# Kernel tuning notes

Measured on AMD Instinct MI355X. Metric: run time of the kernel, lower is better.

## Reference

```python
import jax, jax.numpy as jnp
import numpy as np

N_NODES = 100000
N_EDGES = 1600000
IN_DIM, HID_DIM, OUT_DIM = 128, 256, 512
BN_EPS = 1e-5


def setup_inputs() -> dict:
    key = jax.random.key(0)
    ks = jax.random.split(key, 10)
    x = jax.random.normal(ks[0], (N_NODES, IN_DIM), dtype=jnp.float32)
    edge_index = jax.random.randint(ks[1], (2, N_EDGES), 0, N_NODES, dtype=jnp.int64)
    def lin(k, o, i):
        return jax.random.normal(k, (o, i), dtype=jnp.float32) * (1.0 / np.sqrt(i))
    return {
        "x": x,
        "edge_index": edge_index,
        # SAGEConv 1: in_dim -> hidden_dim (lin_l has bias, lin_r has none)
        "W1l": lin(ks[2], HID_DIM, IN_DIM),
        "b1": jnp.zeros((HID_DIM,), dtype=jnp.float32),
        "W1r": lin(ks[3], HID_DIM, IN_DIM),
        # BatchNorm1d(hidden_dim)
        "gamma": jnp.ones((HID_DIM,), dtype=jnp.float32),
        "beta": jnp.zeros((HID_DIM,), dtype=jnp.float32),
        # SAGEConv 2: hidden_dim -> gnn_out_dim
        "W2l": lin(ks[4], OUT_DIM, HID_DIM),
        "b2": jnp.zeros((OUT_DIM,), dtype=jnp.float32),
        "W2r": lin(ks[5], OUT_DIM, HID_DIM),
    }


def _sage_max(h, src, dst, Wl, b, Wr, n_nodes):
    # gather source features, max-aggregate onto destination nodes
    agg = jax.ops.segment_max(h[src], dst, num_segments=n_nodes)  # [N, D]
    agg = jnp.where(jnp.isneginf(agg), 0.0, agg)  # PyG fills empty segments with 0
    return agg @ Wl.T + b + h @ Wr.T


def reference(x, edge_index, W1l, b1, W1r, gamma, beta, W2l, b2, W2r):
    src, dst = edge_index[0], edge_index[1]
    n = x.shape[0]
    # layer 1: SAGEConv(in_dim, hidden_dim, aggr='max')
    h = _sage_max(x, src, dst, W1l, b1, W1r, n)
    # BatchNorm1d (batch statistics), Dropout is identity in eval; no activation in 'sage' branch
    mean = jnp.mean(h, axis=0)
    var = jnp.var(h, axis=0)
    h = gamma * (h - mean) * jax.lax.rsqrt(var + BN_EPS) + beta
    # layer 2: SAGEConv(hidden_dim, gnn_out_dim, aggr='max')
    out = _sage_max(h, src, dst, W2l, b2, W2r, n)
    return out
```

## Files before the change

kernel.cpp:

```cpp
#include <hip/hip_runtime.h>
#include <hip/hip_bf16.h>
#include <stdint.h>

#define N_NODES 100000
#define N_EDGES 1600000
#define IN_DIM 128
#define HID_DIM 256
#define OUT_DIM 512
#define NBUK 391
#define BCAP 8192
#define EPB 4096

typedef __attribute__((ext_vector_type(4))) float f32x4;
typedef __attribute__((ext_vector_type(8))) short bf16x8;

__device__ __forceinline__ float bf16lo(uint32_t u){ uint32_t b = u << 16; return __builtin_bit_cast(float, b); }
__device__ __forceinline__ float bf16hi(uint32_t u){ uint32_t b = u & 0xffff0000u; return __builtin_bit_cast(float, b); }
__device__ __forceinline__ uint16_t f32_to_bf16(float f){
  uint32_t u = __builtin_bit_cast(uint32_t, f);
  uint32_t r = (u + 0x7fffu + ((u >> 16) & 1u)) >> 16;
  return (uint16_t)r;
}
__device__ __forceinline__ uint32_t pack_bf16_exact(float lo, float hi){
  return (__builtin_bit_cast(uint32_t, hi) & 0xffff0000u) | (__builtin_bit_cast(uint32_t, lo) >> 16);
}
__device__ __forceinline__ uint32_t pack_bf16_rne(float lo, float hi){
  return (uint32_t)f32_to_bf16(lo) | ((uint32_t)f32_to_bf16(hi) << 16);
}
__device__ __forceinline__ void gl2lds16(const void* g, void* l){
  __builtin_amdgcn_global_load_lds(
      (const __attribute__((address_space(1))) uint32_t*)g,
      (__attribute__((address_space(3))) uint32_t*)l, 16, 0, 0);
}

__global__ void k_convx(const float* __restrict__ x, uint16_t* __restrict__ X1x,
                        int* __restrict__ gcur, float* __restrict__ sum,
                        float* __restrict__ sumsq){
  if (blockIdx.x == 12500){
    const int t = threadIdx.x;
    for (int i = t; i < NBUK; i += 256) gcur[i] = i << 13;
    sum[t] = 0.f; sumsq[t] = 0.f;
    return;
  }
  const int idx = blockIdx.x * 256 + threadIdx.x;
  const int n = idx >> 5, q = idx & 31;
  const float4 v = *(const float4*)(x + (long)n * 128 + q * 4);
  ushort4 o;
  o.x = f32_to_bf16(v.x); o.y = f32_to_bf16(v.y);
  o.z = f32_to_bf16(v.z); o.w = f32_to_bf16(v.w);
  *(ushort4*)(X1x + (long)n * 128 + q * 4) = o;
}

__global__ void k_bucket(const int* __restrict__ src, const int* __restrict__ dst,
                         int* __restrict__ gcur, int* __restrict__ ebuk){
  __shared__ int hist[NBUK], curs[NBUK], base[NBUK];
  const int tid = threadIdx.x;
  const int e0 = blockIdx.x * EPB;
  for (int t = tid; t < NBUK; t += 256) hist[t] = 0;
  __syncthreads();
  for (int i = 0; i < EPB; i += 256){
    int e = e0 + i + tid;
    if (e < N_EDGES) atomicAdd(&hist[dst[e] >> 8], 1);
  }
  __syncthreads();
  for (int t = tid; t < NBUK; t += 256){
    int h = hist[t];
    base[t] = h ? atomicAdd(&gcur[t], h) : 0;
    curs[t] = 0;
  }
  __syncthreads();
  for (int i = 0; i < EPB; i += 256){
    int e = e0 + i + tid;
    if (e < N_EDGES){
      int d = dst[e];
      int b = d >> 8;
      int idx = atomicAdd(&curs[b], 1);
      int pos = base[b] + idx;
      if (pos < ((b + 1) << 13))
        ebuk[pos] = ((d & 255) << 17) | src[e];
    }
  }
}

__global__ __launch_bounds__(256)
void k_fillc(const int* __restrict__ gcur, const int* __restrict__ ebuk,
             int* __restrict__ row_start, int* __restrict__ esrc){
  __shared__ int ebuf[BCAP];
  __shared__ int cnt[256];
  __shared__ int wtot[4];
  __shared__ int red[4];
  const int b = blockIdx.x, tid = threadIdx.x, lane = tid & 63, wv = tid >> 6;
  const int nodebase = b << 8;
  const int nodecnt = min(256, N_NODES - nodebase);
  int accb = 0;
  for (int t = tid; t < b; t += 256) accb += gcur[t] - (t << 13);
  #pragma unroll
  for (int d = 32; d > 0; d >>= 1) accb += __shfl_xor(accb, d);
  if (lane == 0) red[wv] = accb;
  int size_b = gcur[b] - (b << 13);
  if (size_b > BCAP) size_b = BCAP;
  cnt[tid] = 0;
  for (int i = tid; i < size_b; i += 256) ebuf[i] = ebuk[(b << 13) + i];
  __syncthreads();
  const int bs = red[0] + red[1] + red[2] + red[3];
  for (int i = tid; i < size_b; i += 256) atomicAdd(&cnt[ebuf[i] >> 17], 1);
  __syncthreads();
  const int c = cnt[tid];
  int v = c;
  #pragma unroll
  for (int d = 1; d < 64; d <<= 1){ int t = __shfl_up(v, d); if (lane >= d) v += t; }
  if (lane == 63) wtot[wv] = v;
  __syncthreads();
  if (tid < 4){
    int t = wtot[tid];
    #pragma unroll
    for (int d = 1; d < 4; d <<= 1){ int u = __shfl_up(t, d); if (tid >= d) t += u; }
    wtot[tid] = t;
  }
  __syncthreads();
  const int excl = (wv ? wtot[wv - 1] : 0) + (v - c);
  if (tid < nodecnt) row_start[nodebase + tid] = bs + excl;
  if (b == NBUK - 1 && tid == 0) row_start[N_NODES] = N_EDGES;
  cnt[tid] = excl;
  __syncthreads();
  for (int i = tid; i < size_b; i += 256){
    int p = ebuf[i];
    int pos = atomicAdd(&cnt[p >> 17], 1);
    esrc[bs + pos] = p & 0x1FFFF;
  }
}

__global__ void k_w1(const float* __restrict__ W1l, const float* __restrict__ W1r,
                     uint16_t* __restrict__ W1cat){
  int idx = blockIdx.x * 256 + threadIdx.x;
  int j = idx >> 8, k = idx & 255;
  float v = (k < 128) ? W1l[j * 128 + k] : W1r[j * 128 + (k - 128)];
  W1cat[idx] = f32_to_bf16(v);
}

__global__ void k_w2(const float* __restrict__ W2l, const float* __restrict__ W2r,
                     const float* __restrict__ b2, const float* __restrict__ sum,
                     const float* __restrict__ sumsq, const float* __restrict__ gamma,
                     const float* __restrict__ beta, uint16_t* __restrict__ W2cat,
                     float* __restrict__ bias2, float* __restrict__ scale_g,
                     float* __restrict__ shift_g){
  __shared__ float sc_s[256], sh_s[256];
  const int tid = threadIdx.x;
  {
    const float inv_n = 1.0f / (float)N_NODES;
    float mean = sum[tid] * inv_n;
    float var = sumsq[tid] * inv_n - mean * mean;
    float sc = gamma[tid] * rsqrtf(var + 1e-5f);
    float sh = beta[tid] - mean * sc;
    sc_s[tid] = sc; sh_s[tid] = sh;
    if (blockIdx.x == 0){ scale_g[tid] = sc; shift_g[tid] = sh; }
  }
  __syncthreads();
  const int wid = (blockIdx.x * 256 + tid) >> 6;
  const int lane = tid & 63;
  float part = 0.f;
  #pragma unroll
  for (int t = 0; t < 4; t++){
    int k = t * 64 + lane;
    float wl = W2l[(long)wid * 256 + k];
    W2cat[(long)wid * 512 + k] = f32_to_bf16(wl);
    float wr = W2r[(long)wid * 256 + k];
    W2cat[(long)wid * 512 + 256 + k] = f32_to_bf16(wr * sc_s[k]);
    part += sh_s[k] * wr;
  }
  #pragma unroll
  for (int d = 32; d > 0; d >>= 1) part += __shfl_xor(part, d);
  if (lane == 0) bias2[wid] = b2[wid] + part;
}

__global__ void k_agg1(const uint32_t* __restrict__ X1x, const int* __restrict__ row_start,
                       const int* __restrict__ esrc, uint32_t* __restrict__ X1agg){
  const int wid = (blockIdx.x * 256 + threadIdx.x) >> 6;
  const int lane = threadIdx.x & 63;
  if (wid >= N_NODES) return;
  const int grp = lane >> 4, li = lane & 15;
  const int s0 = row_start[wid], s1 = row_start[wid + 1];
  float m[8];
  #pragma unroll
  for (int j = 0; j < 8; j++) m[j] = -INFINITY;

  #define ACC1(u)                                        \
    m[0] = fmaxf(m[0], bf16lo(u.x)); m[1] = fmaxf(m[1], bf16hi(u.x)); \
    m[2] = fmaxf(m[2], bf16lo(u.y)); m[3] = fmaxf(m[3], bf16hi(u.y)); \
    m[4] = fmaxf(m[4], bf16lo(u.z)); m[5] = fmaxf(m[5], bf16hi(u.z)); \
    m[6] = fmaxf(m[6], bf16lo(u.w)); m[7] = fmaxf(m[7], bf16hi(u.w));

  int e = s0 + grp;
  for (; e + 12 < s1; e += 16){
    const uint4 ua = *(const uint4*)(X1x + (long)esrc[e] * 64 + li * 4);
    const uint4 ub = *(const uint4*)(X1x + (long)esrc[e + 4] * 64 + li * 4);
    const uint4 uc = *(const uint4*)(X1x + (long)esrc[e + 8] * 64 + li * 4);
    const uint4 ud = *(const uint4*)(X1x + (long)esrc[e + 12] * 64 + li * 4);
    ACC1(ua); ACC1(ub); ACC1(uc); ACC1(ud);
  }
  for (; e < s1; e += 4){
    const uint4 u = *(const uint4*)(X1x + (long)esrc[e] * 64 + li * 4);
    ACC1(u);
  }
  #undef ACC1
  #pragma unroll
  for (int j = 0; j < 8; j++){
    m[j] = fmaxf(m[j], __shfl_xor(m[j], 16));
    m[j] = fmaxf(m[j], __shfl_xor(m[j], 32));
  }
  if (grp == 0){
    uint4 o;
    if (s1 == s0){ o.x = o.y = o.z = o.w = 0u; }
    else {
      o.x = pack_bf16_exact(m[0], m[1]);
      o.y = pack_bf16_exact(m[2], m[3]);
      o.z = pack_bf16_exact(m[4], m[5]);
      o.w = pack_bf16_exact(m[6], m[7]);
    }
    *(uint4*)(X1agg + (long)wid * 64 + li * 4) = o;
  }
}

__global__ void k_agg2(const uint32_t* __restrict__ X2h, const int* __restrict__ row_start,
                       const int* __restrict__ esrc, const float* __restrict__ scale,
                       const float* __restrict__ shift, uint32_t* __restrict__ X2agg){
  const int wid = (blockIdx.x * 256 + threadIdx.x) >> 6;
  const int lane = threadIdx.x & 63;
  if (wid >= N_NODES) return;
  const int half = lane >> 5, li = lane & 31;
  const int c0 = li * 8;
  const float4 sca = *(const float4*)(scale + c0);
  const float4 scb = *(const float4*)(scale + c0 + 4);
  const float4 sha = *(const float4*)(shift + c0);
  const float4 shb = *(const float4*)(shift + c0 + 4);
  const int s0 = row_start[wid], s1 = row_start[wid + 1];
  float m[8];
  #pragma unroll
  for (int j = 0; j < 8; j++) m[j] = -INFINITY;

  #define ACC8(u)                                                   \
    m[0] = fmaxf(m[0], fmaf(bf16lo(u.x), sca.x, sha.x));            \
    m[1] = fmaxf(m[1], fmaf(bf16hi(u.x), sca.y, sha.y));            \
    m[2] = fmaxf(m[2], fmaf(bf16lo(u.y), sca.z, sha.z));            \
    m[3] = fmaxf(m[3], fmaf(bf16hi(u.y), sca.w, sha.w));            \
    m[4] = fmaxf(m[4], fmaf(bf16lo(u.z), scb.x, shb.x));            \
    m[5] = fmaxf(m[5], fmaf(bf16hi(u.z), scb.y, shb.y));            \
    m[6] = fmaxf(m[6], fmaf(bf16lo(u.w), scb.z, shb.z));            \
    m[7] = fmaxf(m[7], fmaf(bf16hi(u.w), scb.w, shb.w));

  int e = s0 + half;
  for (; e + 6 < s1; e += 8){
    const uint4 ua = *(const uint4*)(X2h + (long)esrc[e] * 128 + li * 4);
    const uint4 ub = *(const uint4*)(X2h + (long)esrc[e + 2] * 128 + li * 4);
    const uint4 uc = *(const uint4*)(X2h + (long)esrc[e + 4] * 128 + li * 4);
    const uint4 ud = *(const uint4*)(X2h + (long)esrc[e + 6] * 128 + li * 4);
    ACC8(ua); ACC8(ub); ACC8(uc); ACC8(ud);
  }
  for (; e < s1; e += 2){
    const uint4 u = *(const uint4*)(X2h + (long)esrc[e] * 128 + li * 4);
    ACC8(u);
  }
  #undef ACC8
  #pragma unroll
  for (int j = 0; j < 8; j++) m[j] = fmaxf(m[j], __shfl_xor(m[j], 32));
  if (half == 0){
    uint4 o;
    if (s1 == s0){ o.x = 0u; o.y = 0u; o.z = 0u; o.w = 0u; }
    else {
      o.x = pack_bf16_rne(m[0], m[1]);
      o.y = pack_bf16_rne(m[2], m[3]);
      o.z = pack_bf16_rne(m[4], m[5]);
      o.w = pack_bf16_rne(m[6], m[7]);
    }
    *(uint4*)(X2agg + (long)wid * 128 + li * 4) = o;
  }
}

template<int KT, bool EPI1>
__global__ __launch_bounds__(256, 2)
void k_gemm(const uint16_t* __restrict__ Alo, const uint16_t* __restrict__ Ahi,
            const uint16_t* __restrict__ B, const float* __restrict__ bias,
            uint16_t* __restrict__ outb, float* __restrict__ outf,
            float* __restrict__ sum, float* __restrict__ sumsq)
{
  constexpr int NSTEPS = KT / 64;
  constexpr int HSTEPS = NSTEPS / 2;
  constexpr int NT = EPI1 ? 256 : 512;
  constexpr int NW = NT / 128;
  constexpr int WG = 782 * NW;
  constexpr int PER = (WG + 7) / 8;
  __shared__ uint8_t lds[2][32768];
  const int bid = blockIdx.x;
  const int wgid = (bid & 7) * PER + (bid >> 3);
  if (wgid >= WG) return;
  const int mblk = wgid / NW, nblk = wgid % NW;
  const int tid = threadIdx.x, lane = tid & 63, wv = tid >> 6;
  const int wvm = wv >> 1, wvn = wv & 1;

  f32x4 acc[4][4] = {};

  const int srow = wv * 32 + (lane >> 3);
  const int skb  = (lane & 7) * 16;

  const uint8_t* asrc_lo[4];
  const uint8_t* asrc_hi[4];
  const uint8_t* bsrc[4];
  #pragma unroll
  for (int i = 0; i < 4; i++){
    int row = srow + i * 8;
    int kbsw = skb ^ ((row & 7) << 4);
    long grow = (long)mblk * 128 + row;
    if (grow > N_NODES - 1) grow = N_NODES - 1;
    asrc_lo[i] = (const uint8_t*)Alo + grow * KT + kbsw;
    asrc_hi[i] = (const uint8_t*)Ahi + grow * KT + kbsw;
    bsrc[i] = (const uint8_t*)B + ((long)nblk * 128 + row) * (KT * 2) + kbsw;
  }

  #define STAGE(ks, buf)                                                     \
    _Pragma("unroll")                                                        \
    for (int i = 0; i < 4; i++)                                              \
      gl2lds16((ks) < HSTEPS ? asrc_lo[i] + (ks) * 128                       \
                             : asrc_hi[i] + ((ks) - HSTEPS) * 128,           \
               &lds[buf][(wv * 4 + i) * 1024]);                              \
    _Pragma("unroll")                                                        \
    for (int i = 0; i < 4; i++)                                              \
      gl2lds16(bsrc[i] + (ks) * 128, &lds[buf][16384 + (wv * 4 + i) * 1024]);

  STAGE(0, 0);

  #pragma unroll
  for (int ks = 0; ks < NSTEPS; ++ks){
    const int cur = ks & 1;
    if (ks + 1 < NSTEPS){
      STAGE(ks + 1, cur ^ 1);
      asm volatile("s_waitcnt vmcnt(8)" ::: "memory");
    } else {
      asm volatile("s_waitcnt vmcnt(0)" ::: "memory");
    }
    __builtin_amdgcn_s_barrier();
    asm volatile("" ::: "memory");

    const uint8_t* ldsA = &lds[cur][0];
    const uint8_t* ldsB = &lds[cur][16384];
    bf16x8 af[4][2], bfr[4][2];
    #pragma unroll
    for (int m = 0; m < 4; m++){
      int row = wvm * 64 + m * 16 + (lane & 15);
      #pragma unroll
      for (int kk = 0; kk < 2; kk++){
        int kb = kk * 64 + (lane >> 4) * 16;
        af[m][kk] = *(const bf16x8*)(ldsA + row * 128 + (kb ^ ((row & 7) << 4)));
      }
    }
    #pragma unroll
    for (int n = 0; n < 4; n++){
      int row = wvn * 64 + n * 16 + (lane & 15);
      #pragma unroll
      for (int kk = 0; kk < 2; kk++){
        int kb = kk * 64 + (lane >> 4) * 16;
        bfr[n][kk] = *(const bf16x8*)(ldsB + row * 128 + (kb ^ ((row & 7) << 4)));
      }
    }
    #pragma unroll
    for (int kk = 0; kk < 2; kk++)
      #pragma unroll
      for (int m = 0; m < 4; m++)
        #pragma unroll
        for (int n = 0; n < 4; n++)
          acc[m][n] = __builtin_amdgcn_mfma_f32_16x16x32_bf16(af[m][kk], bfr[n][kk], acc[m][n], 0, 0, 0);

    asm volatile("" ::: "memory");
    __builtin_amdgcn_s_barrier();
    asm volatile("" ::: "memory");
  }
  #undef STAGE

  const int rgrp = (lane >> 4) * 4;
  #pragma unroll
  for (int n = 0; n < 4; n++){
    const int col = nblk * 128 + wvn * 64 + n * 16 + (lane & 15);
    const float bv = bias[col];
    float s1v = 0.f, s2v = 0.f;
    #pragma unroll
    for (int m = 0; m < 4; m++){
      const int rowb = mblk * 128 + wvm * 64 + m * 16 + rgrp;
      f32x4 v = acc[m][n];
      #pragma unroll
      for (int j = 0; j < 4; j++){
        const int row = rowb + j;
        const float h = v[j] + bv;
        if (row < N_NODES){
          if (EPI1){
            outb[(long)row * NT + col] = f32_to_bf16(h);
            s1v += h; s2v += h * h;
          } else {
            __builtin_nontemporal_store(h, &outf[(long)row * NT + col]);
          }
        }
      }
    }
    if (EPI1){
      s1v += __shfl_xor(s1v, 16); s1v += __shfl_xor(s1v, 32);
      s2v += __shfl_xor(s2v, 16); s2v += __shfl_xor(s2v, 32);
      if (lane < 16){
        atomicAdd(&sum[col], s1v);
        atomicAdd(&sumsq[col], s2v);
      }
    }
  }
}

extern "C" void kernel_launch(void* const* d_in, const int* in_sizes, int n_in,
                              void* d_out, int out_size, void* d_ws, size_t ws_size,
                              hipStream_t stream){
  const float* x     = (const float*)d_in[0];
  const int*   ei    = (const int*)d_in[1];
  const float* W1l   = (const float*)d_in[2];
  const float* b1    = (const float*)d_in[3];
  const float* W1r   = (const float*)d_in[4];
  const float* gamma = (const float*)d_in[5];
  const float* beta  = (const float*)d_in[6];
  const float* W2l   = (const float*)d_in[7];
  const float* b2    = (const float*)d_in[8];
  const float* W2r   = (const float*)d_in[9];
  const int* esrc_in = ei;
  const int* edst_in = ei + N_EDGES;

  uint8_t* ws = (uint8_t*)d_ws;
  uint16_t* X1agg    = (uint16_t*)(ws + 0);
  uint16_t* X1x      = (uint16_t*)(ws + 25600000);
  uint16_t* X2agg    = (uint16_t*)(ws + 51200000);
  uint16_t* X2h      = (uint16_t*)(ws + 102400000);
  int* ebuk          = (int*)(ws + 51200000);
  int* esrc          = (int*)(ws + 153600000);
  int* row_start     = (int*)(ws + 160000000);
  int* gcur          = (int*)(ws + 160402176);
  uint16_t* W1cat    = (uint16_t*)(ws + 160800256);
  uint16_t* W2cat    = (uint16_t*)(ws + 160931328);
  float* bias2       = (float*)(ws + 161455616);
  float* sum         = (float*)(ws + 161457664);
  float* sumsq       = (float*)(ws + 161458688);
  float* scale       = (float*)(ws + 161459712);
  float* shift       = (float*)(ws + 161460736);

  hipLaunchKernelGGL(k_convx, dim3(12501), dim3(256), 0, stream, x, X1x, gcur, sum, sumsq);
  hipLaunchKernelGGL(k_bucket, dim3((N_EDGES + EPB - 1) / EPB), dim3(256), 0, stream,
                     esrc_in, edst_in, gcur, ebuk);
  hipLaunchKernelGGL(k_fillc, dim3(NBUK), dim3(256), 0, stream,
                     gcur, ebuk, row_start, esrc);

  hipLaunchKernelGGL(k_w1, dim3(256), dim3(256), 0, stream, W1l, W1r, W1cat);
  hipLaunchKernelGGL(k_agg1, dim3(25000), dim3(256), 0, stream,
                     (const uint32_t*)X1x, row_start, esrc, (uint32_t*)X1agg);

  hipLaunchKernelGGL((k_gemm<256, true>), dim3(1568), dim3(256), 0, stream,
                     X1agg, X1x, W1cat, b1, X2h, (float*)nullptr, sum, sumsq);

  hipLaunchKernelGGL(k_w2, dim3(128), dim3(256), 0, stream,
                     W2l, W2r, b2, sum, sumsq, gamma, beta, W2cat, bias2, scale, shift);

  hipLaunchKernelGGL(k_agg2, dim3(25000), dim3(256), 0, stream,
                     (const uint32_t*)X2h, row_start, esrc, scale, shift, (uint32_t*)X2agg);

  hipLaunchKernelGGL((k_gemm<512, false>), dim3(3128), dim3(256), 0, stream,
                     X2agg, X2h, W2cat, bias2, (uint16_t*)nullptr, (float*)d_out,
                     (float*)nullptr, (float*)nullptr);
}
```

Measured before the change: 396.9 us.

## Drop GEMM double buffering for single LDS buffer and higher occupancy

The GEMM kernel moves from a double-buffered LDS prefetch pipeline to a single 32 KB buffer with plain syncthreads around each stage. Launch bounds rise from 2 to 4 blocks per CU, and fragment loads are restructured per k-substep to cut register pressure. The aim is to hide memory latency through more resident waves rather than software pipelining, at the cost of losing in-block overlap of loads and MFMA. The edge-bucketing kernel also halves edges per block, which launches more blocks.

```diff
diff --git a/kernel.cpp b/kernel.cpp
--- a/kernel.cpp
+++ b/kernel.cpp
@@ -9,7 +9,7 @@
 #define OUT_DIM 512
 #define NBUK 391
 #define BCAP 8192
-#define EPB 4096
+#define EPB 2048
 
 typedef __attribute__((ext_vector_type(4))) float f32x4;
 typedef __attribute__((ext_vector_type(8))) short bf16x8;
@@ -277,7 +277,7 @@
 }
 
 template<int KT, bool EPI1>
-__global__ __launch_bounds__(256, 2)
+__global__ __launch_bounds__(256, 4)
 void k_gemm(const uint16_t* __restrict__ Alo, const uint16_t* __restrict__ Ahi,
             const uint16_t* __restrict__ B, const float* __restrict__ bias,
             uint16_t* __restrict__ outb, float* __restrict__ outf,
@@ -289,7 +289,7 @@
   constexpr int NW = NT / 128;
   constexpr int WG = 782 * NW;
   constexpr int PER = (WG + 7) / 8;
-  __shared__ uint8_t lds[2][32768];
+  __shared__ uint8_t lds[32768];
   const int bid = blockIdx.x;
   const int wgid = (bid & 7) * PER + (bid >> 3);
   if (wgid >= WG) return;
@@ -316,62 +316,45 @@
     bsrc[i] = (const uint8_t*)B + ((long)nblk * 128 + row) * (KT * 2) + kbsw;
   }
 
-  #define STAGE(ks, buf)                                                     \
+  #define STAGE(ks)                                                          \
     _Pragma("unroll")                                                        \
     for (int i = 0; i < 4; i++)                                              \
-      gl2lds16((ks) < HSTEPS ? asrc_lo[i] + (ks) * 128                       \
-                             : asrc_hi[i] + ((ks) - HSTEPS) * 128,           \
-               &lds[buf][(wv * 4 + i) * 1024]);                              \
+      gl2lds16((ks) < HSTEPS ? asrc_lo[i] + (long)(ks) * 128                 \
+                             : asrc_hi[i] + (long)((ks) - HSTEPS) * 128,     \
+               &lds[(wv * 4 + i) * 1024]);                                   \
     _Pragma("unroll")                                                        \
     for (int i = 0; i < 4; i++)                                              \
-      gl2lds16(bsrc[i] + (ks) * 128, &lds[buf][16384 + (wv * 4 + i) * 1024]);
-
-  STAGE(0, 0);
+      gl2lds16(bsrc[i] + (long)(ks) * 128,                                   \
+               &lds[16384 + (wv * 4 + i) * 1024]);
 
   #pragma unroll
   for (int ks = 0; ks < NSTEPS; ++ks){
-    const int cur = ks & 1;
-    if (ks + 1 < NSTEPS){
-      STAGE(ks + 1, cur ^ 1);
-      asm volatile("s_waitcnt vmcnt(8)" ::: "memory");
-    } else {
-      asm volatile("s_waitcnt vmcnt(0)" ::: "memory");
-    }
-    __builtin_amdgcn_s_barrier();
-    asm volatile("" ::: "memory");
-
-    const uint8_t* ldsA = &lds[cur][0];
-    const uint8_t* ldsB = &lds[cur][16384];
-    bf16x8 af[4][2], bfr[4][2];
+    if (ks) __syncthreads();
+    STAGE(ks);
+    __syncthreads();
+
+    const uint8_t* ldsA = &lds[0];
+    const uint8_t* ldsB = &lds[16384];
     #pragma unroll
-    for (int m = 0; m < 4; m++){
-      int row = wvm * 64 + m * 16 + (lane & 15);
+    for (int kk = 0; kk < 2; kk++){
+      const int kb = kk * 64 + (lane >> 4) * 16;
+      bf16x8 af[4], bfr[4];
       #pragma unroll
-      for (int kk = 0; kk < 2; kk++){
-        int kb = kk * 64 + (lane >> 4) * 16;
-        af[m][kk] = *(const bf16x8*)(ldsA + row * 128 + (kb ^ ((row & 7) << 4)));
+      for (int m = 0; m < 4; m++){
+        int row = wvm * 64 + m * 16 + (lane & 15);
+        af[m] = *(const bf16x8*)(ldsA + row * 128 + (kb ^ ((row & 7) << 4)));
       }
-    }
-    #pragma unroll
-    for (int n = 0; n < 4; n++){
-      int row = wvn * 64 + n * 16 + (lane & 15);
       #pragma unroll
-      for (int kk = 0; kk < 2; kk++){
-        int kb = kk * 64 + (lane >> 4) * 16;
-        bfr[n][kk] = *(const bf16x8*)(ldsB + row * 128 + (kb ^ ((row & 7) << 4)));
+      for (int n = 0; n < 4; n++){
+        int row = wvn * 64 + n * 16 + (lane & 15);
+        bfr[n] = *(const bf16x8*)(ldsB + row * 128 + (kb ^ ((row & 7) << 4)));
       }
-    }
-    #pragma unroll
-    for (int kk = 0; kk < 2; kk++)
       #pragma unroll
       for (int m = 0; m < 4; m++)
         #pragma unroll
         for (int n = 0; n < 4; n++)
-          acc[m][n] = __builtin_amdgcn_mfma_f32_16x16x32_bf16(af[m][kk], bfr[n][kk], acc[m][n], 0, 0, 0);
-
-    asm volatile("" ::: "memory");
-    __builtin_amdgcn_s_barrier();
-    asm volatile("" ::: "memory");
+          acc[m][n] = __builtin_amdgcn_mfma_f32_16x16x32_bf16(af[m], bfr[n], acc[m][n], 0, 0, 0);
+    }
   }
   #undef STAGE
 
@@ -444,7 +427,7 @@
   float* shift       = (float*)(ws + 161460736);
 
   hipLaunchKernelGGL(k_convx, dim3(12501), dim3(256), 0, stream, x, X1x, gcur, sum, sumsq);
-  hipLaunchKernelGGL(k_bucket, dim3((N_EDGES + EPB - 1) / EPB), dim3(256), 0, stream,
+  hipLaunchKernelGGL(k_bucket, dim3(N_EDGES / EPB + 1), dim3(256), 0, stream,
                      esrc_in, edst_in, gcur, ebuk);
   hipLaunchKernelGGL(k_fillc, dim3(NBUK), dim3(256), 0, stream,
                      gcur, ebuk, row_start, esrc);
```

Measured after the change: 393.2 us. No clear change (-0.9%).
